# Performance work log

Measured on AMD Instinct MI355X. Metric: run time of the kernel, lower is better.

Reference implementation:

```python
import jax, jax.numpy as jnp
import numpy as np

B, H, W, D = 8, 64, 64, 256   # batch, grid rows, grid cols, q_size==c_size
N = 1024                      # number of query/alignment points
R_WIN, C_WIN = 1, 2           # hardcoded window half-sizes from the module


def setup_inputs() -> dict:
    key = jax.random.key(0)
    k1, k2, k3, k4 = jax.random.split(key, 4)
    q = jax.random.normal(k1, (B, H, W, D), jnp.float32)
    c_t = jax.random.normal(k2, (B, N, D), jnp.float32)
    # float positions inside the grid: row in [0,H-1), col in [0,W-1)
    p_t = jax.random.uniform(k3, (B, N, 2), jnp.float32) * jnp.array([H - 1, W - 1], jnp.float32)
    W_a = jax.random.normal(k4, (D, D), jnp.float32) / np.sqrt(D)  # nn.Linear(q_size->c_size) weight [c,q]
    return {"q": q, "c_t": c_t, "p_t": p_t, "W_a": W_a}


def reference(q, c_t, p_t, W_a):
    Bq, Hh, Ww, Dd = q.shape
    rows, cols = Hh + 1, Ww + 1
    # ConstantPad2d((1,0,1,0), nan) on channels-first layout == pad top row & left col with NaN
    q_pad = jnp.pad(q.transpose(0, 3, 1, 2), ((0, 0), (0, 0), (1, 0), (1, 0)),
                    constant_values=jnp.nan)                      # [B,D,rows,cols]
    p0 = p_t[..., 0].astype(jnp.int32)
    p1 = p_t[..., 1].astype(jnp.int32)
    r = jnp.clip(p0[..., None] + jnp.arange(-R_WIN, R_WIN + 1) + 1, 0, rows) % rows  # [B,N,2R+1]
    c = jnp.clip(p1[..., None] + jnp.arange(-C_WIN, C_WIN + 1) + 1, 0, cols) % cols  # [B,N,2C+1]
    # flattened window indices, i (row offset) major, j (col offset) minor
    idx = (r[..., :, None] * cols + c[..., None, :]).reshape(Bq, r.shape[1], -1)     # [B,N,K]
    K = idx.shape[-1]
    q_flat = q_pad.reshape(Bq, Dd, rows * cols).transpose(0, 2, 1)                   # [B,rows*cols,D]
    qg = jnp.take_along_axis(q_flat, idx.reshape(Bq, -1, 1), axis=1)
    qg = qg.reshape(Bq, idx.shape[1], K, Dd)                                          # [B,N,K,D]
    nan_loc = jnp.isnan(qg[..., 0])                                                   # [B,N,K]
    qg = jnp.where(nan_loc[..., None], 0.0, qg)
    # Gaussian decay around the (float) predicted position
    rexp = jnp.exp(-2.0 * ((jnp.clip(r.astype(q.dtype) - 1, 0, None) - p_t[..., 0:1]) / R_WIN) ** 2)
    cexp = jnp.exp(-2.0 * ((jnp.clip(c.astype(q.dtype) - 1, 0, None) - p_t[..., 1:2]) / C_WIN) ** 2)
    expw = (rexp[..., :, None] * cexp[..., None, :]).reshape(Bq, r.shape[1], K)       # [B,N,K]
    # score: (W_a qg) . c_t per (b,n)
    Wa = jnp.einsum('bnkd,cd->bnkc', qg, W_a)
    a_t = jnp.einsum('bnkc,bnc->bnk', Wa, c_t)
    a_t = jnp.where(nan_loc, -jnp.inf, a_t)
    W_attn = jax.nn.softmax(a_t, axis=2) * expw
    return jnp.einsum('bnk,bnkd->bnd', W_attn, qg)                                    # [B,N,D]
```

## Files before the change

### kernel.cpp

```cpp
#include <hip/hip_runtime.h>
#include <math.h>

#define BATCH   8
#define HGRID   64
#define WGRID   64
#define DDIM    256
#define NPTS    1024
#define ROWS    65
#define COLS    65
#define KWIN    15
#define BN      (BATCH*NPTS)

#define PIDS_PER_BLK 16
#define THREADS      512
#define NREG         9
#define NLDS         6

typedef __attribute__((ext_vector_type(8))) short bf16x8;
typedef __attribute__((ext_vector_type(4))) float f32x4;

__device__ __forceinline__ void gload_lds16(const float* src, float* dst) {
    __builtin_amdgcn_global_load_lds(
        (const __attribute__((address_space(1))) unsigned int*)src,
        (__attribute__((address_space(3))) unsigned int*)dst, 16, 0, 0);
}

__global__ __launch_bounds__(THREADS, 4) void fused_local_attn(
        const float* __restrict__ q,
        const float* __restrict__ c_t,
        const float* __restrict__ p_t,
        const float* __restrict__ W,
        float* __restrict__ out) {

    __shared__ __align__(16) float smem[NLDS * DDIM * 8];
    float (*Pr)[DDIM] = reinterpret_cast<float (*)[DDIM]>(smem);

    const int t    = threadIdx.x;
    const int w    = t >> 6;
    const int lane = t & 63;
    const int l15  = lane & 15;
    const int g    = lane >> 4;
    const int bid  = blockIdx.x;
    const int wk   = (bid & 7) * 64 + (bid >> 3);
    const int pid0 = wk * PIDS_PER_BLK;
    const int dq   = w * 32;
    float* qsw = smem + w * (NLDS * DDIM);

    f32x4 acc0 = (f32x4)0.f;
    f32x4 acc1 = (f32x4)0.f;

    const float* ap  = &c_t[(size_t)(pid0 + l15) * DDIM + g * 8];
    const float* wp0 = &W[(size_t)(g * 8) * DDIM + dq + l15];
    const float* wp1 = wp0 + 16;

    #pragma unroll 2
    for (int kt = 0; kt < 8; ++kt) {
        const float4 a01 = *reinterpret_cast<const float4*>(ap + kt * 32);
        const float4 a23 = *reinterpret_cast<const float4*>(ap + kt * 32 + 4);
        const float af[8] = {a01.x, a01.y, a01.z, a01.w, a23.x, a23.y, a23.z, a23.w};
        union { bf16x8 v; unsigned u[4]; } AH, AL;
        #pragma unroll
        for (int i = 0; i < 4; ++i) {
            const unsigned u0 = __float_as_uint(af[2 * i]);
            const unsigned u1 = __float_as_uint(af[2 * i + 1]);
            AH.u[i] = __builtin_amdgcn_perm(u1, u0, 0x07060302u);
            const float l0 = af[2 * i]     - __uint_as_float(u0 & 0xFFFF0000u);
            const float l1 = af[2 * i + 1] - __uint_as_float(u1 & 0xFFFF0000u);
            AL.u[i] = __builtin_amdgcn_perm(__float_as_uint(l1), __float_as_uint(l0),
                                            0x07060302u);
        }

        #pragma unroll
        for (int df = 0; df < 2; ++df) {
            const float* wp = (df == 0) ? wp0 : wp1;
            float bf[8];
            #pragma unroll
            for (int i = 0; i < 8; ++i)
                bf[i] = wp[(size_t)(kt * 32 + i) * DDIM];
            union { bf16x8 v; unsigned u[4]; } BH, BL;
            #pragma unroll
            for (int i = 0; i < 4; ++i) {
                const unsigned u0 = __float_as_uint(bf[2 * i]);
                const unsigned u1 = __float_as_uint(bf[2 * i + 1]);
                BH.u[i] = __builtin_amdgcn_perm(u1, u0, 0x07060302u);
                const float l0 = bf[2 * i]     - __uint_as_float(u0 & 0xFFFF0000u);
                const float l1 = bf[2 * i + 1] - __uint_as_float(u1 & 0xFFFF0000u);
                BL.u[i] = __builtin_amdgcn_perm(__float_as_uint(l1), __float_as_uint(l0),
                                                0x07060302u);
            }
            f32x4 a = (df == 0) ? acc0 : acc1;
            a = __builtin_amdgcn_mfma_f32_16x16x32_bf16(AH.v, BH.v, a, 0, 0, 0);
            a = __builtin_amdgcn_mfma_f32_16x16x32_bf16(AH.v, BL.v, a, 0, 0, 0);
            a = __builtin_amdgcn_mfma_f32_16x16x32_bf16(AL.v, BH.v, a, 0, 0, 0);
            if (df == 0) acc0 = a; else acc1 = a;
        }
    }

    #pragma unroll
    for (int r = 0; r < 4; ++r) {
        Pr[g * 4 + r][dq +  0 + l15] = acc0[r];
        Pr[g * 4 + r][dq + 16 + l15] = acc1[r];
    }
    __syncthreads();

    const float4 prA = *reinterpret_cast<const float4*>(&Pr[w * 2 + 0][lane * 4]);
    const float4 prB = *reinterpret_cast<const float4*>(&Pr[w * 2 + 1][lane * 4]);
    __syncthreads();

    const int pidA = pid0 + w * 2 + 0;
    const int pidB = pid0 + w * 2 + 1;
    const int bb   = pidA >> 10;

    const float2 posA = *reinterpret_cast<const float2*>(&p_t[pidA * 2]);
    const float2 posB = *reinterpret_cast<const float2*>(&p_t[pidB * 2]);

    float reA[3], ceA[5];
    int rowA[3], colA[5];
    {
        const int p0 = (int)posA.x, p1 = (int)posA.y;
        #pragma unroll
        for (int i = 0; i < 3; ++i) {
            int rr = p0 + i;
            rr = rr > ROWS ? ROWS : rr;
            rr = (rr == ROWS) ? 0 : rr;
            rowA[i] = rr;
            const float rf = (float)(rr - 1 > 0 ? rr - 1 : 0);
            const float dr = rf - posA.x;
            reA[i] = __expf(-2.0f * dr * dr);
        }
        #pragma unroll
        for (int j = 0; j < 5; ++j) {
            int cc = p1 + j - 1;
            cc = cc < 0 ? 0 : (cc > COLS ? COLS : cc);
            cc = (cc == COLS) ? 0 : cc;
            colA[j] = cc;
            const float cf = (float)(cc - 1 > 0 ? cc - 1 : 0);
            const float dc = (cf - posA.y) * 0.5f;
            ceA[j] = __expf(-2.0f * dc * dc);
        }
    }
    int rowB[3], colB[5];
    {
        const int p0 = (int)posB.x, p1 = (int)posB.y;
        #pragma unroll
        for (int i = 0; i < 3; ++i) {
            int rr = p0 + i;
            rr = rr > ROWS ? ROWS : rr;
            rr = (rr == ROWS) ? 0 : rr;
            rowB[i] = rr;
        }
        #pragma unroll
        for (int j = 0; j < 5; ++j) {
            int cc = p1 + j - 1;
            cc = cc < 0 ? 0 : (cc > COLS ? COLS : cc);
            cc = (cc == COLS) ? 0 : cc;
            colB[j] = cc;
        }
    }

    float4 qgA[NREG];
    unsigned vmA = 0;
    #pragma unroll
    for (int k = 0; k < KWIN; ++k) {
        const int i = k / 5, j = k % 5;
        const int rr = rowA[i], cc = colA[j];
        const bool valid = (rr != 0) && (cc != 0);
        const float* src =
            &q[((size_t)((bb * HGRID + rr - 1) * WGRID + cc - 1)) * DDIM + lane * 4];
        if (k < NREG) {
            float4 v = make_float4(0.f, 0.f, 0.f, 0.f);
            if (valid) v = *reinterpret_cast<const float4*>(src);
            qgA[k] = v;
        } else {
            if (valid) gload_lds16(src, &qsw[(k - NREG) * DDIM]);
        }
        if (valid) vmA |= (1u << k);
    }

    __builtin_amdgcn_sched_barrier(0);

    float4 qgB[NREG];
    unsigned vmB = 0;
    #pragma unroll
    for (int k = 0; k < NREG; ++k) {
        const int i = k / 5, j = k % 5;
        const int rr = rowB[i], cc = colB[j];
        const bool valid = (rr != 0) && (cc != 0);
        float4 v = make_float4(0.f, 0.f, 0.f, 0.f);
        if (valid) {
            v = *reinterpret_cast<const float4*>(
                &q[((size_t)((bb * HGRID + rr - 1) * WGRID + cc - 1)) * DDIM + lane * 4]);
            vmB |= (1u << k);
        }
        qgB[k] = v;
    }
    #pragma unroll
    for (int k = NREG; k < KWIN; ++k) {
        const int i = k / 5, j = k % 5;
        if ((rowB[i] != 0) && (colB[j] != 0)) vmB |= (1u << k);
    }

    asm volatile("s_waitcnt vmcnt(9)" ::: "memory");
    #pragma unroll
    for (int k = 0; k < NREG; ++k)
        asm volatile("" : "+v"(qgA[k].x), "+v"(qgA[k].y), "+v"(qgA[k].z), "+v"(qgA[k].w));

    {
        float score[KWIN];
        #pragma unroll
        for (int k = 0; k < NREG; ++k) {
            const float4 v = qgA[k];
            score[k] = fmaf(v.x, prA.x, fmaf(v.y, prA.y, fmaf(v.z, prA.z, v.w * prA.w)));
        }
        #pragma unroll
        for (int k = NREG; k < KWIN; ++k) {
            const float4 v =
                *reinterpret_cast<const float4*>(&qsw[(k - NREG) * DDIM + lane * 4]);
            score[k] = fmaf(v.x, prA.x, fmaf(v.y, prA.y, fmaf(v.z, prA.z, v.w * prA.w)));
        }
        #pragma unroll
        for (int k = 0; k < KWIN; ++k) {
            float s = score[k];
            #pragma unroll
            for (int off = 32; off; off >>= 1) s += __shfl_xor(s, off, 64);
            score[k] = ((vmA >> k) & 1u) ? s : -INFINITY;
        }
        float mx = score[0];
        #pragma unroll
        for (int k = 1; k < KWIN; ++k) mx = fmaxf(mx, score[k]);
        float sum = 0.f;
        #pragma unroll
        for (int k = 0; k < KWIN; ++k) {
            const float e = __expf(score[k] - mx);
            score[k] = e;
            sum += e;
        }
        const float inv = 1.0f / sum;

        float ox = 0.f, oy = 0.f, oz = 0.f, ow = 0.f;
        #pragma unroll
        for (int k = 0; k < KWIN; ++k) {
            const int i = k / 5, j = k % 5;
            const float wk2 = score[k] * inv * reA[i] * ceA[j];
            if (k < NREG) {
                ox = fmaf(wk2, qgA[k].x, ox);
                oy = fmaf(wk2, qgA[k].y, oy);
                oz = fmaf(wk2, qgA[k].z, oz);
                ow = fmaf(wk2, qgA[k].w, ow);
            } else if ((vmA >> k) & 1u) {
                const float4 v =
                    *reinterpret_cast<const float4*>(&qsw[(k - NREG) * DDIM + lane * 4]);
                ox = fmaf(wk2, v.x, ox);
                oy = fmaf(wk2, v.y, oy);
                oz = fmaf(wk2, v.z, oz);
                ow = fmaf(wk2, v.w, ow);
            }
        }
        *reinterpret_cast<float4*>(&out[(size_t)pidA * DDIM + lane * 4]) =
            make_float4(ox, oy, oz, ow);
    }

    asm volatile("s_waitcnt lgkmcnt(0)" ::: "memory");
    __builtin_amdgcn_sched_barrier(0);
    #pragma unroll
    for (int k = NREG; k < KWIN; ++k) {
        const int i = k / 5, j = k % 5;
        const int rr = rowB[i], cc = colB[j];
        if ((rr != 0) && (cc != 0)) {
            gload_lds16(&q[((size_t)((bb * HGRID + rr - 1) * WGRID + cc - 1)) * DDIM
                           + lane * 4],
                        &qsw[(k - NREG) * DDIM]);
        }
    }

    float reB[3], ceB[5];
    {
        #pragma unroll
        for (int i = 0; i < 3; ++i) {
            const int rr = rowB[i];
            const float rf = (float)(rr - 1 > 0 ? rr - 1 : 0);
            const float dr = rf - posB.x;
            reB[i] = __expf(-2.0f * dr * dr);
        }
        #pragma unroll
        for (int j = 0; j < 5; ++j) {
            const int cc = colB[j];
            const float cf = (float)(cc - 1 > 0 ? cc - 1 : 0);
            const float dc = (cf - posB.y) * 0.5f;
            ceB[j] = __expf(-2.0f * dc * dc);
        }
    }

    asm volatile("s_waitcnt vmcnt(0)" ::: "memory");
    #pragma unroll
    for (int k = 0; k < NREG; ++k)
        asm volatile("" : "+v"(qgB[k].x), "+v"(qgB[k].y), "+v"(qgB[k].z), "+v"(qgB[k].w));

    {
        float score[KWIN];
        #pragma unroll
        for (int k = 0; k < NREG; ++k) {
            const float4 v = qgB[k];
            score[k] = fmaf(v.x, prB.x, fmaf(v.y, prB.y, fmaf(v.z, prB.z, v.w * prB.w)));
        }
        #pragma unroll
        for (int k = NREG; k < KWIN; ++k) {
            const float4 v =
                *reinterpret_cast<const float4*>(&qsw[(k - NREG) * DDIM + lane * 4]);
            score[k] = fmaf(v.x, prB.x, fmaf(v.y, prB.y, fmaf(v.z, prB.z, v.w * prB.w)));
        }
        #pragma unroll
        for (int k = 0; k < KWIN; ++k) {
            float s = score[k];
            #pragma unroll
            for (int off = 32; off; off >>= 1) s += __shfl_xor(s, off, 64);
            score[k] = ((vmB >> k) & 1u) ? s : -INFINITY;
        }
        float mx = score[0];
        #pragma unroll
        for (int k = 1; k < KWIN; ++k) mx = fmaxf(mx, score[k]);
        float sum = 0.f;
        #pragma unroll
        for (int k = 0; k < KWIN; ++k) {
            const float e = __expf(score[k] - mx);
            score[k] = e;
            sum += e;
        }
        const float inv = 1.0f / sum;

        float ox = 0.f, oy = 0.f, oz = 0.f, ow = 0.f;
        #pragma unroll
        for (int k = 0; k < KWIN; ++k) {
            const int i = k / 5, j = k % 5;
            const float wk2 = score[k] * inv * reB[i] * ceB[j];
            if (k < NREG) {
                ox = fmaf(wk2, qgB[k].x, ox);
                oy = fmaf(wk2, qgB[k].y, oy);
                oz = fmaf(wk2, qgB[k].z, oz);
                ow = fmaf(wk2, qgB[k].w, ow);
            } else if ((vmB >> k) & 1u) {
                const float4 v =
                    *reinterpret_cast<const float4*>(&qsw[(k - NREG) * DDIM + lane * 4]);
                ox = fmaf(wk2, v.x, ox);
                oy = fmaf(wk2, v.y, oy);
                oz = fmaf(wk2, v.z, oz);
                ow = fmaf(wk2, v.w, ow);
            }
        }
        *reinterpret_cast<float4*>(&out[(size_t)pidB * DDIM + lane * 4]) =
            make_float4(ox, oy, oz, ow);
    }
}

extern "C" void kernel_launch(void* const* d_in, const int* in_sizes, int n_in,
                              void* d_out, int out_size, void* d_ws, size_t ws_size,
                              hipStream_t stream) {
    const float* q   = (const float*)d_in[0];
    const float* c_t = (const float*)d_in[1];
    const float* p_t = (const float*)d_in[2];
    const float* W_a = (const float*)d_in[3];
    float* out = (float*)d_out;

    fused_local_attn<<<BN / PIDS_PER_BLK, THREADS, 0, stream>>>(q, c_t, p_t, W_a, out);
}
```

Baseline: 35.55 us.

## Replace LDS-staged window gathers with register loads and clamped unconditional addresses

The 6 of 15 window rows per point that were staged through LDS via global_load_lds are now loaded straight into registers, so all 15 window vectors for point A live in VGPRs. Invalid (NaN-pad) window entries now load a clamped valid address instead of branching, and rely on the valid mask for -inf scores. For point B, 4 loads are prefetched before point A's compute and the other 11 are issued after it. The LDS buffer shrinks to a padded 16x260 tile and the second __syncthreads is removed. This raises register pressure under the 512-thread, 4-block launch bound, which risks spilling or lower occupancy.

```diff
diff --git a/kernel.cpp b/kernel.cpp
--- a/kernel.cpp
+++ b/kernel.cpp
@@ -13,17 +13,11 @@
 
 #define PIDS_PER_BLK 16
 #define THREADS      512
-#define NREG         9
-#define NLDS         6
+#define PR_PITCH     260
+#define NPRE         4
 
 typedef __attribute__((ext_vector_type(8))) short bf16x8;
 typedef __attribute__((ext_vector_type(4))) float f32x4;
-
-__device__ __forceinline__ void gload_lds16(const float* src, float* dst) {
-    __builtin_amdgcn_global_load_lds(
-        (const __attribute__((address_space(1))) unsigned int*)src,
-        (__attribute__((address_space(3))) unsigned int*)dst, 16, 0, 0);
-}
 
 __global__ __launch_bounds__(THREADS, 4) void fused_local_attn(
         const float* __restrict__ q,
@@ -32,8 +26,7 @@
         const float* __restrict__ W,
         float* __restrict__ out) {
 
-    __shared__ __align__(16) float smem[NLDS * DDIM * 8];
-    float (*Pr)[DDIM] = reinterpret_cast<float (*)[DDIM]>(smem);
+    __shared__ __align__(16) float Pr[PIDS_PER_BLK][PR_PITCH];
 
     const int t    = threadIdx.x;
     const int w    = t >> 6;
@@ -44,7 +37,6 @@
     const int wk   = (bid & 7) * 64 + (bid >> 3);
     const int pid0 = wk * PIDS_PER_BLK;
     const int dq   = w * 32;
-    float* qsw = smem + w * (NLDS * DDIM);
 
     f32x4 acc0 = (f32x4)0.f;
     f32x4 acc1 = (f32x4)0.f;
@@ -103,18 +95,14 @@
     }
     __syncthreads();
 
+    const int pidA = pid0 + w * 2 + 0;
+    const int pidB = pid0 + w * 2 + 1;
+    const int b    = pidA >> 10;
     const float4 prA = *reinterpret_cast<const float4*>(&Pr[w * 2 + 0][lane * 4]);
     const float4 prB = *reinterpret_cast<const float4*>(&Pr[w * 2 + 1][lane * 4]);
-    __syncthreads();
-
-    const int pidA = pid0 + w * 2 + 0;
-    const int pidB = pid0 + w * 2 + 1;
-    const int bb   = pidA >> 10;
-
     const float2 posA = *reinterpret_cast<const float2*>(&p_t[pidA * 2]);
     const float2 posB = *reinterpret_cast<const float2*>(&p_t[pidB * 2]);
 
-    float reA[3], ceA[5];
     int rowA[3], colA[5];
     {
         const int p0 = (int)posA.x, p1 = (int)posA.y;
@@ -122,23 +110,45 @@
         for (int i = 0; i < 3; ++i) {
             int rr = p0 + i;
             rr = rr > ROWS ? ROWS : rr;
-            rr = (rr == ROWS) ? 0 : rr;
-            rowA[i] = rr;
-            const float rf = (float)(rr - 1 > 0 ? rr - 1 : 0);
-            const float dr = rf - posA.x;
-            reA[i] = __expf(-2.0f * dr * dr);
+            rowA[i] = (rr == ROWS) ? 0 : rr;
         }
         #pragma unroll
         for (int j = 0; j < 5; ++j) {
             int cc = p1 + j - 1;
             cc = cc < 0 ? 0 : (cc > COLS ? COLS : cc);
-            cc = (cc == COLS) ? 0 : cc;
-            colA[j] = cc;
-            const float cf = (float)(cc - 1 > 0 ? cc - 1 : 0);
-            const float dc = (cf - posA.y) * 0.5f;
-            ceA[j] = __expf(-2.0f * dc * dc);
-        }
-    }
+            colA[j] = (cc == COLS) ? 0 : cc;
+        }
+    }
+
+    float4 qgA[KWIN];
+    unsigned vmA = 0;
+    #pragma unroll
+    for (int k = 0; k < KWIN; ++k) {
+        const int i = k / 5, j = k % 5;
+        const int rr = rowA[i], cc = colA[j];
+        if ((rr != 0) && (cc != 0)) vmA |= (1u << k);
+        const int rrc = rr ? rr : 1;
+        const int ccc = cc ? cc : 1;
+        qgA[k] = *reinterpret_cast<const float4*>(
+            &q[((size_t)((b * HGRID + rrc - 1) * WGRID + ccc - 1)) * DDIM + lane * 4]);
+    }
+
+    float reA[3], ceA[5];
+    #pragma unroll
+    for (int i = 0; i < 3; ++i) {
+        const float rf = (float)(rowA[i] - 1 > 0 ? rowA[i] - 1 : 0);
+        const float dr = rf - posA.x;
+        reA[i] = __expf(-2.0f * dr * dr);
+    }
+    #pragma unroll
+    for (int j = 0; j < 5; ++j) {
+        const float cf = (float)(colA[j] - 1 > 0 ? colA[j] - 1 : 0);
+        const float dc = (cf - posA.y) * 0.5f;
+        ceA[j] = __expf(-2.0f * dc * dc);
+    }
+
+    __builtin_amdgcn_sched_barrier(0);
+
     int rowB[3], colB[5];
     {
         const int p0 = (int)posB.x, p1 = (int)posB.y;
@@ -146,76 +156,41 @@
         for (int i = 0; i < 3; ++i) {
             int rr = p0 + i;
             rr = rr > ROWS ? ROWS : rr;
-            rr = (rr == ROWS) ? 0 : rr;
-            rowB[i] = rr;
+            rowB[i] = (rr == ROWS) ? 0 : rr;
         }
         #pragma unroll
         for (int j = 0; j < 5; ++j) {
             int cc = p1 + j - 1;
             cc = cc < 0 ? 0 : (cc > COLS ? COLS : cc);
-            cc = (cc == COLS) ? 0 : cc;
-            colB[j] = cc;
-        }
-    }
-
-    float4 qgA[NREG];
-    unsigned vmA = 0;
+            colB[j] = (cc == COLS) ? 0 : cc;
+        }
+    }
+    unsigned vmB = 0;
     #pragma unroll
     for (int k = 0; k < KWIN; ++k) {
         const int i = k / 5, j = k % 5;
-        const int rr = rowA[i], cc = colA[j];
-        const bool valid = (rr != 0) && (cc != 0);
-        const float* src =
-            &q[((size_t)((bb * HGRID + rr - 1) * WGRID + cc - 1)) * DDIM + lane * 4];
-        if (k < NREG) {
-            float4 v = make_float4(0.f, 0.f, 0.f, 0.f);
-            if (valid) v = *reinterpret_cast<const float4*>(src);
-            qgA[k] = v;
-        } else {
-            if (valid) gload_lds16(src, &qsw[(k - NREG) * DDIM]);
-        }
-        if (valid) vmA |= (1u << k);
-    }
-
-    __builtin_amdgcn_sched_barrier(0);
-
-    float4 qgB[NREG];
-    unsigned vmB = 0;
-    #pragma unroll
-    for (int k = 0; k < NREG; ++k) {
+        if ((rowB[i] != 0) && (colB[j] != 0)) vmB |= (1u << k);
+    }
+    float4 qgBpre[NPRE];
+    #pragma unroll
+    for (int k = 0; k < NPRE; ++k) {
         const int i = k / 5, j = k % 5;
-        const int rr = rowB[i], cc = colB[j];
-        const bool valid = (rr != 0) && (cc != 0);
-        float4 v = make_float4(0.f, 0.f, 0.f, 0.f);
-        if (valid) {
-            v = *reinterpret_cast<const float4*>(
-                &q[((size_t)((bb * HGRID + rr - 1) * WGRID + cc - 1)) * DDIM + lane * 4]);
-            vmB |= (1u << k);
-        }
-        qgB[k] = v;
-    }
-    #pragma unroll
-    for (int k = NREG; k < KWIN; ++k) {
-        const int i = k / 5, j = k % 5;
-        if ((rowB[i] != 0) && (colB[j] != 0)) vmB |= (1u << k);
-    }
-
-    asm volatile("s_waitcnt vmcnt(9)" ::: "memory");
-    #pragma unroll
-    for (int k = 0; k < NREG; ++k)
+        const int rrc = rowB[i] ? rowB[i] : 1;
+        const int ccc = colB[j] ? colB[j] : 1;
+        qgBpre[k] = *reinterpret_cast<const float4*>(
+            &q[((size_t)((b * HGRID + rrc - 1) * WGRID + ccc - 1)) * DDIM + lane * 4]);
+    }
+
+    asm volatile("s_waitcnt vmcnt(" "4" ")" ::: "memory");
+    #pragma unroll
+    for (int k = 0; k < KWIN; ++k)
         asm volatile("" : "+v"(qgA[k].x), "+v"(qgA[k].y), "+v"(qgA[k].z), "+v"(qgA[k].w));
 
     {
         float score[KWIN];
         #pragma unroll
-        for (int k = 0; k < NREG; ++k) {
+        for (int k = 0; k < KWIN; ++k) {
             const float4 v = qgA[k];
-            score[k] = fmaf(v.x, prA.x, fmaf(v.y, prA.y, fmaf(v.z, prA.z, v.w * prA.w)));
-        }
-        #pragma unroll
-        for (int k = NREG; k < KWIN; ++k) {
-            const float4 v =
-                *reinterpret_cast<const float4*>(&qsw[(k - NREG) * DDIM + lane * 4]);
             score[k] = fmaf(v.x, prA.x, fmaf(v.y, prA.y, fmaf(v.z, prA.z, v.w * prA.w)));
         }
         #pragma unroll
@@ -236,77 +211,61 @@
             sum += e;
         }
         const float inv = 1.0f / sum;
-
         float ox = 0.f, oy = 0.f, oz = 0.f, ow = 0.f;
         #pragma unroll
         for (int k = 0; k < KWIN; ++k) {
             const int i = k / 5, j = k % 5;
             const float wk2 = score[k] * inv * reA[i] * ceA[j];
-            if (k < NREG) {
-                ox = fmaf(wk2, qgA[k].x, ox);
-                oy = fmaf(wk2, qgA[k].y, oy);
-                oz = fmaf(wk2, qgA[k].z, oz);
-                ow = fmaf(wk2, qgA[k].w, ow);
-            } else if ((vmA >> k) & 1u) {
-                const float4 v =
-                    *reinterpret_cast<const float4*>(&qsw[(k - NREG) * DDIM + lane * 4]);
-                ox = fmaf(wk2, v.x, ox);
-                oy = fmaf(wk2, v.y, oy);
-                oz = fmaf(wk2, v.z, oz);
-                ow = fmaf(wk2, v.w, ow);
-            }
+            ox = fmaf(wk2, qgA[k].x, ox);
+            oy = fmaf(wk2, qgA[k].y, oy);
+            oz = fmaf(wk2, qgA[k].z, oz);
+            ow = fmaf(wk2, qgA[k].w, ow);
         }
         *reinterpret_cast<float4*>(&out[(size_t)pidA * DDIM + lane * 4]) =
             make_float4(ox, oy, oz, ow);
     }
 
-    asm volatile("s_waitcnt lgkmcnt(0)" ::: "memory");
     __builtin_amdgcn_sched_barrier(0);
-    #pragma unroll
-    for (int k = NREG; k < KWIN; ++k) {
+
+    float4 qgBr[KWIN - NPRE];
+    #pragma unroll
+    for (int k = NPRE; k < KWIN; ++k) {
         const int i = k / 5, j = k % 5;
-        const int rr = rowB[i], cc = colB[j];
-        if ((rr != 0) && (cc != 0)) {
-            gload_lds16(&q[((size_t)((bb * HGRID + rr - 1) * WGRID + cc - 1)) * DDIM
-                           + lane * 4],
-                        &qsw[(k - NREG) * DDIM]);
-        }
+        const int rrc = rowB[i] ? rowB[i] : 1;
+        const int ccc = colB[j] ? colB[j] : 1;
+        qgBr[k - NPRE] = *reinterpret_cast<const float4*>(
+            &q[((size_t)((b * HGRID + rrc - 1) * WGRID + ccc - 1)) * DDIM + lane * 4]);
     }
 
     float reB[3], ceB[5];
-    {
-        #pragma unroll
-        for (int i = 0; i < 3; ++i) {
-            const int rr = rowB[i];
-            const float rf = (float)(rr - 1 > 0 ? rr - 1 : 0);
-            const float dr = rf - posB.x;
-            reB[i] = __expf(-2.0f * dr * dr);
-        }
-        #pragma unroll
-        for (int j = 0; j < 5; ++j) {
-            const int cc = colB[j];
-            const float cf = (float)(cc - 1 > 0 ? cc - 1 : 0);
-            const float dc = (cf - posB.y) * 0.5f;
-            ceB[j] = __expf(-2.0f * dc * dc);
-        }
+    #pragma unroll
+    for (int i = 0; i < 3; ++i) {
+        const float rf = (float)(rowB[i] - 1 > 0 ? rowB[i] - 1 : 0);
+        const float dr = rf - posB.x;
+        reB[i] = __expf(-2.0f * dr * dr);
+    }
+    #pragma unroll
+    for (int j = 0; j < 5; ++j) {
+        const float cf = (float)(colB[j] - 1 > 0 ? colB[j] - 1 : 0);
+        const float dc = (cf - posB.y) * 0.5f;
+        ceB[j] = __expf(-2.0f * dc * dc);
     }
 
     asm volatile("s_waitcnt vmcnt(0)" ::: "memory");
     #pragma unroll
-    for (int k = 0; k < NREG; ++k)
-        asm volatile("" : "+v"(qgB[k].x), "+v"(qgB[k].y), "+v"(qgB[k].z), "+v"(qgB[k].w));
+    for (int k = 0; k < NPRE; ++k)
+        asm volatile("" : "+v"(qgBpre[k].x), "+v"(qgBpre[k].y),
+                          "+v"(qgBpre[k].z), "+v"(qgBpre[k].w));
+    #pragma unroll
+    for (int k = 0; k < KWIN - NPRE; ++k)
+        asm volatile("" : "+v"(qgBr[k].x), "+v"(qgBr[k].y),
+                          "+v"(qgBr[k].z), "+v"(qgBr[k].w));
 
     {
         float score[KWIN];
         #pragma unroll
-        for (int k = 0; k < NREG; ++k) {
-            const float4 v = qgB[k];
-            score[k] = fmaf(v.x, prB.x, fmaf(v.y, prB.y, fmaf(v.z, prB.z, v.w * prB.w)));
-        }
-        #pragma unroll
-        for (int k = NREG; k < KWIN; ++k) {
-            const float4 v =
-                *reinterpret_cast<const float4*>(&qsw[(k - NREG) * DDIM + lane * 4]);
+        for (int k = 0; k < KWIN; ++k) {
+            const float4 v = (k < NPRE) ? qgBpre[k] : qgBr[k - NPRE];
             score[k] = fmaf(v.x, prB.x, fmaf(v.y, prB.y, fmaf(v.z, prB.z, v.w * prB.w)));
         }
         #pragma unroll
@@ -327,25 +286,16 @@
             sum += e;
         }
         const float inv = 1.0f / sum;
-
         float ox = 0.f, oy = 0.f, oz = 0.f, ow = 0.f;
         #pragma unroll
         for (int k = 0; k < KWIN; ++k) {
             const int i = k / 5, j = k % 5;
             const float wk2 = score[k] * inv * reB[i] * ceB[j];
-            if (k < NREG) {
-                ox = fmaf(wk2, qgB[k].x, ox);
-                oy = fmaf(wk2, qgB[k].y, oy);
-                oz = fmaf(wk2, qgB[k].z, oz);
-                ow = fmaf(wk2, qgB[k].w, ow);
-            } else if ((vmB >> k) & 1u) {
-                const float4 v =
-                    *reinterpret_cast<const float4*>(&qsw[(k - NREG) * DDIM + lane * 4]);
-                ox = fmaf(wk2, v.x, ox);
-                oy = fmaf(wk2, v.y, oy);
-                oz = fmaf(wk2, v.z, oz);
-                ow = fmaf(wk2, v.w, ow);
-            }
+            const float4 v = (k < NPRE) ? qgBpre[k] : qgBr[k - NPRE];
+            ox = fmaf(wk2, v.x, ox);
+            oy = fmaf(wk2, v.y, oy);
+            oz = fmaf(wk2, v.z, oz);
+            ow = fmaf(wk2, v.w, ow);
         }
         *reinterpret_cast<float4*>(&out[(size_t)pidB * DDIM + lane * 4]) =
             make_float4(ox, oy, oz, ow);
```

Result: slower. 38.39 us (+8.0%).
